# Optimization experiments

Hardware: AMD Instinct MI355X
Metric: run time of the kernel (lower is better)

The kernel has to match this reference:

```python
import jax, jax.numpy as jnp
import numpy as np

B, S, D, H, DK, F, K = 8, 1024, 512, 8, 64, 2048, 31
EPS = 1e-5


def _ln(x, g, b):
    m = jnp.mean(x, -1, keepdims=True)
    v = jnp.mean((x - m) ** 2, -1, keepdims=True)
    return (x - m) * jax.lax.rsqrt(v + EPS) * g + b


def _ff(x, w1, b1, w2, b2):
    return jnp.maximum(x @ w1 + b1, 0.0) @ w2 + b2


def setup_inputs() -> dict:
    key = jax.random.key(0)
    ks = jax.random.split(key, 16)
    w = lambda k, shape: jax.random.normal(k, shape, dtype=jnp.float32) * 0.02
    inp = {"x": jax.random.normal(ks[0], (B, S, D), dtype=jnp.float32)}
    for name in ["norm1", "norm2", "norm3", "norm4", "conv_ln"]:
        inp[name + "_g"] = jnp.ones((D,), jnp.float32)
        inp[name + "_b"] = jnp.zeros((D,), jnp.float32)
    # feed-forward 1 and 2
    inp["ff1_w1"] = w(ks[1], (D, F)); inp["ff1_b1"] = jnp.zeros((F,), jnp.float32)
    inp["ff1_w2"] = w(ks[2], (F, D)); inp["ff1_b2"] = jnp.zeros((D,), jnp.float32)
    inp["ff2_w1"] = w(ks[3], (D, F)); inp["ff2_b1"] = jnp.zeros((F,), jnp.float32)
    inp["ff2_w2"] = w(ks[4], (F, D)); inp["ff2_b2"] = jnp.zeros((D,), jnp.float32)
    # attention projections ([in, out] layout)
    inp["wq"] = w(ks[5], (D, D)); inp["bq"] = jnp.zeros((D,), jnp.float32)
    inp["wk"] = w(ks[6], (D, D)); inp["bk"] = jnp.zeros((D,), jnp.float32)
    inp["wv"] = w(ks[7], (D, D)); inp["bv"] = jnp.zeros((D,), jnp.float32)
    inp["wo"] = w(ks[8], (D, D)); inp["bo"] = jnp.zeros((D,), jnp.float32)
    # convolution module
    inp["pw1_w"] = w(ks[9], (D, 2 * D)); inp["pw1_b"] = jnp.zeros((2 * D,), jnp.float32)
    inp["dw_w"] = w(ks[10], (D, 1, K)); inp["dw_b"] = jnp.zeros((D,), jnp.float32)
    inp["bn_g"] = jnp.ones((D,), jnp.float32); inp["bn_b"] = jnp.zeros((D,), jnp.float32)
    inp["bn_mean"] = jnp.zeros((D,), jnp.float32); inp["bn_var"] = jnp.ones((D,), jnp.float32)
    inp["pw2_w"] = w(ks[11], (D, D)); inp["pw2_b"] = jnp.zeros((D,), jnp.float32)
    return inp


def _forward(x, norm1_g, norm1_b, norm2_g, norm2_b, norm3_g, norm3_b, norm4_g, norm4_b,
             ff1_w1, ff1_b1, ff1_w2, ff1_b2, wq, bq, wk, bk, wv, bv, wo, bo,
             conv_ln_g, conv_ln_b, pw1_w, pw1_b, dw_w, dw_b,
             bn_g, bn_b, bn_mean, bn_var, pw2_w, pw2_b,
             ff2_w1, ff2_b1, ff2_w2, ff2_b2):
    b, s, _ = x.shape
    # half-step FF1
    x = x + 0.5 * _ff(_ln(x, norm1_g, norm1_b), ff1_w1, ff1_b1, ff1_w2, ff1_b2)
    # multi-head self-attention (pre-norm)
    h = _ln(x, norm2_g, norm2_b)
    q = (h @ wq + bq).reshape(b, s, H, DK)
    k = (h @ wk + bk).reshape(b, s, H, DK)
    v = (h @ wv + bv).reshape(b, s, H, DK)
    scores = jnp.einsum("bqhd,bkhd->bhqk", q, k) / jnp.sqrt(jnp.asarray(DK, x.dtype))
    attn = jax.nn.softmax(scores, axis=-1)
    o = jnp.einsum("bhqk,bkhd->bqhd", attn, v).reshape(b, s, D)
    x = x + (o @ wo + bo)
    # convolution module (pre-norm)
    h = _ln(x, norm3_g, norm3_b)
    h = _ln(h, conv_ln_g, conv_ln_b)
    h = h @ pw1_w + pw1_b                                 # [B,S,2D] pointwise conv1
    h = h[..., :D] * jax.nn.sigmoid(h[..., D:])           # GLU over channels
    h = h.transpose(0, 2, 1)                              # [B,D,S]
    h = jax.lax.conv_general_dilated(
        h, dw_w, window_strides=(1,), padding=((K // 2, K // 2),),
        feature_group_count=D, dimension_numbers=("NCH", "OIH", "NCH")) + dw_b[:, None]
    h = (h - bn_mean[:, None]) * jax.lax.rsqrt(bn_var + EPS)[:, None] * bn_g[:, None] + bn_b[:, None]
    h = h * jax.nn.sigmoid(h)                             # SiLU
    h = jnp.einsum("bcl,co->bol", h, pw2_w) + pw2_b[:, None]
    x = x + h.transpose(0, 2, 1)
    # half-step FF2
    x = x + 0.5 * _ff(_ln(x, norm4_g, norm4_b), ff2_w1, ff2_b1, ff2_w2, ff2_b2)
    return x


def reference(x, norm1_g, norm1_b, norm2_g, norm2_b, norm3_g, norm3_b, norm4_g, norm4_b,
              conv_ln_g, conv_ln_b, ff1_w1, ff1_b1, ff1_w2, ff1_b2,
              ff2_w1, ff2_b1, ff2_w2, ff2_b2, wq, bq, wk, bk, wv, bv, wo, bo,
              pw1_w, pw1_b, dw_w, dw_b, bn_g, bn_b, bn_mean, bn_var, pw2_w, pw2_b):
    return _forward(x, norm1_g, norm1_b, norm2_g, norm2_b, norm3_g, norm3_b, norm4_g, norm4_b,
                    ff1_w1, ff1_b1, ff1_w2, ff1_b2, wq, bq, wk, bk, wv, bv, wo, bo,
                    conv_ln_g, conv_ln_b, pw1_w, pw1_b, dw_w, dw_b,
                    bn_g, bn_b, bn_mean, bn_var, pw2_w, pw2_b,
                    ff2_w1, ff2_b1, ff2_w2, ff2_b2)
```

## Files before the change

### kernel.cpp

```cpp
#include <hip/hip_runtime.h>
#include <math.h>

#define TOK    8192
#define DMODEL 512
#define FDIM   2048
#define NH     8
#define DKH    64
#define SEQ    1024
#define BATCH  8
#define KCONV  31
#define LN_EPS 1e-5f

typedef __attribute__((ext_vector_type(8))) short bf16x8;
typedef __attribute__((ext_vector_type(4))) float f32x4;
typedef unsigned short ushort_t;

#define AS1 __attribute__((address_space(1)))
#define AS3 __attribute__((address_space(3)))

__device__ __forceinline__ float sigf(float x) { return 1.0f / (1.0f + __expf(-x)); }

__device__ __forceinline__ unsigned short f2bf(float f) {
  unsigned u = __float_as_uint(f);
  u = u + 0x7fffu + ((u >> 16) & 1u);
  return (unsigned short)(u >> 16);
}
__device__ __forceinline__ unsigned pk2(float a, float b) {
  return (unsigned)f2bf(a) | ((unsigned)f2bf(b) << 16);
}
__device__ __forceinline__ float bf2f(ushort_t u) {
  return __uint_as_float((unsigned)u << 16);
}

__device__ __forceinline__ void xcd_swizzle(int gx, int* bx, int* by) {
  const int nwg = gx * (int)gridDim.y;
  const int cpx = nwg >> 3;
  const int bid = (*by) * gx + (*bx);
  const int wg = (bid & 7) * cpx + (bid >> 3);
  *bx = wg % gx;
  *by = wg / gx;
}

struct WJob { const float* src; ushort_t* dst; int K, N, t0; };
struct WJobs {
  WJob j[10];
  int misc_t0;
  const float* dww; const float* bq; const float* bk; const float* bv;
  float* wTc; float* bcat;
};

__global__ __launch_bounds__(256) void wcast_all(WJobs jobs) {
  __shared__ float tile[32][33];
  const int t = blockIdx.x;
  const int tx = threadIdx.x, ty = threadIdx.y;
  if (t >= jobs.misc_t0) {
    const int idx = (t - jobs.misc_t0) * 256 + ty * 32 + tx;
    if (idx < DMODEL * KCONV) {
      const int d = idx / KCONV, k = idx % KCONV;
      jobs.wTc[k * DMODEL + d] = jobs.dww[idx];
    } else if (idx < DMODEL * KCONV + 3 * DMODEL) {
      const int c = idx - DMODEL * KCONV;
      jobs.bcat[c] = (c < DMODEL) ? jobs.bq[c]
                    : (c < 2 * DMODEL ? jobs.bk[c - DMODEL] : jobs.bv[c - 2 * DMODEL]);
    }
    return;
  }
  int i = 0;
#pragma unroll
  for (int k = 1; k < 10; ++k) if (t >= jobs.j[k].t0) i = k;
  const WJob jb = jobs.j[i];
  const int local = t - jb.t0;
  const int ntx = jb.N >> 5;
  const int bx = (local % ntx) * 32, by = (local / ntx) * 32;
#pragma unroll
  for (int r = 0; r < 32; r += 8)
    tile[ty + r][tx] = jb.src[(size_t)(by + ty + r) * jb.N + bx + tx];
  __syncthreads();
#pragma unroll
  for (int r = 0; r < 32; r += 8)
    jb.dst[(size_t)(bx + ty + r) * jb.K + by + tx] = f2bf(tile[tx][ty + r]);
}

template <bool OBF>
__global__ __launch_bounds__(256) void ln_kernel(const float* __restrict__ in,
                                                 const float* __restrict__ g,
                                                 const float* __restrict__ b,
                                                 void* __restrict__ outp) {
  const int wave = threadIdx.x >> 6, lane = threadIdx.x & 63;
  const size_t row = (size_t)blockIdx.x * 4 + wave;
  const float* p = in + row * DMODEL + lane * 8;
  const float4 v0 = *(const float4*)p;
  const float4 v1 = *(const float4*)(p + 4);
  float s  = v0.x + v0.y + v0.z + v0.w + v1.x + v1.y + v1.z + v1.w;
  float ss = v0.x*v0.x + v0.y*v0.y + v0.z*v0.z + v0.w*v0.w
           + v1.x*v1.x + v1.y*v1.y + v1.z*v1.z + v1.w*v1.w;
#pragma unroll
  for (int m = 1; m < 64; m <<= 1) { s += __shfl_xor(s, m); ss += __shfl_xor(ss, m); }
  const float mean = s * (1.0f / DMODEL);
  const float var  = ss * (1.0f / DMODEL) - mean * mean;
  const float rstd = rsqrtf(var + LN_EPS);
  const float4 g0 = *(const float4*)(g + lane * 8);
  const float4 g1 = *(const float4*)(g + lane * 8 + 4);
  const float4 bb0 = *(const float4*)(b + lane * 8);
  const float4 bb1 = *(const float4*)(b + lane * 8 + 4);
  float o[8];
  o[0] = (v0.x - mean) * rstd * g0.x + bb0.x;
  o[1] = (v0.y - mean) * rstd * g0.y + bb0.y;
  o[2] = (v0.z - mean) * rstd * g0.z + bb0.z;
  o[3] = (v0.w - mean) * rstd * g0.w + bb0.w;
  o[4] = (v1.x - mean) * rstd * g1.x + bb1.x;
  o[5] = (v1.y - mean) * rstd * g1.y + bb1.y;
  o[6] = (v1.z - mean) * rstd * g1.z + bb1.z;
  o[7] = (v1.w - mean) * rstd * g1.w + bb1.w;
  if (OBF) {
    uint4 pkv;
    pkv.x = pk2(o[0], o[1]); pkv.y = pk2(o[2], o[3]);
    pkv.z = pk2(o[4], o[5]); pkv.w = pk2(o[6], o[7]);
    *(uint4*)((ushort_t*)outp + row * DMODEL + lane * 8) = pkv;
  } else {
    float4 a, c;
    a.x = o[0]; a.y = o[1]; a.z = o[2]; a.w = o[3];
    c.x = o[4]; c.y = o[5]; c.z = o[6]; c.w = o[7];
    float* q = (float*)outp + row * DMODEL + lane * 8;
    *(float4*)q = a;
    *(float4*)(q + 4) = c;
  }
}

__global__ __launch_bounds__(256) void ln2_kernel(const float* __restrict__ in,
                                                  const float* __restrict__ g1,
                                                  const float* __restrict__ b1,
                                                  const float* __restrict__ g2,
                                                  const float* __restrict__ b2,
                                                  ushort_t* __restrict__ outp) {
  const int wave = threadIdx.x >> 6, lane = threadIdx.x & 63;
  const size_t row = (size_t)blockIdx.x * 4 + wave;
  const float* p = in + row * DMODEL + lane * 8;
  float v[8];
  {
    const float4 v0 = *(const float4*)p;
    const float4 v1 = *(const float4*)(p + 4);
    v[0]=v0.x; v[1]=v0.y; v[2]=v0.z; v[3]=v0.w;
    v[4]=v1.x; v[5]=v1.y; v[6]=v1.z; v[7]=v1.w;
  }
  float s = 0.f, ss = 0.f;
#pragma unroll
  for (int e = 0; e < 8; ++e) { s += v[e]; ss += v[e]*v[e]; }
#pragma unroll
  for (int m = 1; m < 64; m <<= 1) { s += __shfl_xor(s, m); ss += __shfl_xor(ss, m); }
  float mean = s * (1.0f / DMODEL);
  float rstd = rsqrtf(ss * (1.0f / DMODEL) - mean * mean + LN_EPS);
  const float4 ga = *(const float4*)(g1 + lane * 8);
  const float4 gb = *(const float4*)(g1 + lane * 8 + 4);
  const float4 ba = *(const float4*)(b1 + lane * 8);
  const float4 bb = *(const float4*)(b1 + lane * 8 + 4);
  const float gg1[8] = {ga.x,ga.y,ga.z,ga.w,gb.x,gb.y,gb.z,gb.w};
  const float bb1[8] = {ba.x,ba.y,ba.z,ba.w,bb.x,bb.y,bb.z,bb.w};
#pragma unroll
  for (int e = 0; e < 8; ++e) v[e] = (v[e] - mean) * rstd * gg1[e] + bb1[e];
  s = 0.f; ss = 0.f;
#pragma unroll
  for (int e = 0; e < 8; ++e) { s += v[e]; ss += v[e]*v[e]; }
#pragma unroll
  for (int m = 1; m < 64; m <<= 1) { s += __shfl_xor(s, m); ss += __shfl_xor(ss, m); }
  mean = s * (1.0f / DMODEL);
  rstd = rsqrtf(ss * (1.0f / DMODEL) - mean * mean + LN_EPS);
  const float4 gc = *(const float4*)(g2 + lane * 8);
  const float4 gd = *(const float4*)(g2 + lane * 8 + 4);
  const float4 bc = *(const float4*)(b2 + lane * 8);
  const float4 bd = *(const float4*)(b2 + lane * 8 + 4);
  const float gg2[8] = {gc.x,gc.y,gc.z,gc.w,gd.x,gd.y,gd.z,gd.w};
  const float bb2[8] = {bc.x,bc.y,bc.z,bc.w,bd.x,bd.y,bd.z,bd.w};
  float o[8];
#pragma unroll
  for (int e = 0; e < 8; ++e) o[e] = (v[e] - mean) * rstd * gg2[e] + bb2[e];
  uint4 pkv;
  pkv.x = pk2(o[0], o[1]); pkv.y = pk2(o[2], o[3]);
  pkv.z = pk2(o[4], o[5]); pkv.w = pk2(o[6], o[7]);
  *(uint4*)(outp + row * DMODEL + lane * 8) = pkv;
}

template <int ACT, bool QSC>
__global__ __launch_bounds__(512, 2) void gemm256(const ushort_t* __restrict__ A,
                                                  const ushort_t* __restrict__ Bt,
                                                  const float* __restrict__ bias,
                                                  ushort_t* __restrict__ Cout,
                                                  int N) {
  __shared__ ushort_t lds[65536];
  const int t = threadIdx.x;
  const int l = t & 63;
  const int wid = t >> 6;
  const int wm = wid >> 2, wn = wid & 3;
  int bx = blockIdx.x, by = blockIdx.y;
  xcd_swizzle(gridDim.x, &bx, &by);
  const int m0 = by * 256, n0 = bx * 256;
  const int K = 512;

  f32x4 acc[8][4];
#pragma unroll
  for (int m = 0; m < 8; ++m)
#pragma unroll
    for (int n = 0; n < 4; ++n) acc[m][n] = (f32x4){0.f, 0.f, 0.f, 0.f};

  const int srow = t >> 3;
  const int schunk = (t & 7) ^ ((t >> 3) & 7);

#define STAGE_A(TAU, C_, I_)                                                    \
  __builtin_amdgcn_global_load_lds(                                             \
      (const AS1 unsigned*)(A + (size_t)(m0 + (I_) * 64 + srow) * K +           \
                            (TAU) * 64 + schunk * 8),                           \
      (AS3 unsigned*)(lds + (C_) * 16384 + ((I_) * 512 + t) * 8), 16, 0, 0)
#define STAGE_B(TAU, C_, I_)                                                    \
  __builtin_amdgcn_global_load_lds(                                             \
      (const AS1 unsigned*)(Bt + (size_t)(n0 + (I_) * 64 + srow) * K +          \
                            (TAU) * 64 + schunk * 8),                           \
      (AS3 unsigned*)(lds + 32768 + (C_) * 16384 + ((I_) * 512 + t) * 8), 16, 0, 0)

#pragma unroll
  for (int i = 0; i < 4; ++i) STAGE_B(0, 0, i);
#pragma unroll
  for (int i = 0; i < 4; ++i) STAGE_A(0, 0, i);
#pragma unroll
  for (int i = 0; i < 4; ++i) STAGE_B(1, 1, i);
  STAGE_A(1, 1, 0);
  STAGE_A(1, 1, 2);
  asm volatile("s_waitcnt vmcnt(6)" ::: "memory");
  __builtin_amdgcn_s_barrier();

  const int arow = (l & 15);
  const int kch0 = (l >> 4);
  bf16x8 bfr[2][4];

  for (int it = 0; it < 4; ++it) {
    const bool stg = (it < 3);
#pragma unroll
    for (int h = 0; h < 2; ++h) {
      const int c = h;
#pragma unroll
      for (int p = 0; p < 4; ++p) {
        bf16x8 afr[2][2];
#pragma unroll
        for (int m2 = 0; m2 < 2; ++m2)
#pragma unroll
          for (int ks = 0; ks < 2; ++ks) {
            const int row = wm * 128 + (2 * p + m2) * 16 + arow;
            const int ch = (ks * 4 + kch0) ^ (row & 7);
            afr[m2][ks] = *(const bf16x8*)(lds + c * 16384 + row * 64 + ch * 8);
          }
        if (p == 0) {
#pragma unroll
          for (int nr = 0; nr < 4; ++nr)
#pragma unroll
            for (int ks = 0; ks < 2; ++ks) {
              const int row = wn * 64 + nr * 16 + arow;
              const int ch = (ks * 4 + kch0) ^ (row & 7);
              bfr[ks][nr] = *(const bf16x8*)(lds + 32768 + c * 16384 + row * 64 + ch * 8);
            }
        }
        if (p == 0) {
          if (h == 0 || stg) {
            STAGE_A(2 * it + h + 1, c ^ 1, 1);
            STAGE_A(2 * it + h + 1, c ^ 1, 3);
          }
        } else if (p == 1) {
          if (stg) {
#pragma unroll
            for (int i = 0; i < 4; ++i) STAGE_B(2 * it + h + 2, c, i);
          }
        } else if (p == 2) {
          if (stg) {
            STAGE_A(2 * it + h + 2, c, 0);
            STAGE_A(2 * it + h + 2, c, 2);
          }
        }
        __builtin_amdgcn_s_barrier();
        __builtin_amdgcn_s_setprio(1);
#pragma unroll
        for (int ks = 0; ks < 2; ++ks)
#pragma unroll
          for (int m2 = 0; m2 < 2; ++m2)
#pragma unroll
            for (int nr = 0; nr < 4; ++nr)
              acc[2 * p + m2][nr] = __builtin_amdgcn_mfma_f32_16x16x32_bf16(
                  afr[m2][ks], bfr[ks][nr], acc[2 * p + m2][nr], 0, 0, 0);
        __builtin_amdgcn_s_setprio(0);
        if (p == 3) {
          if (h == 0) {
            if (stg) asm volatile("s_waitcnt vmcnt(6)" ::: "memory");
            else     asm volatile("s_waitcnt vmcnt(0)" ::: "memory");
          } else if (stg) {
            asm volatile("s_waitcnt vmcnt(6)" ::: "memory");
          }
        }
        __builtin_amdgcn_s_barrier();
      }
    }
  }
#undef STAGE_A
#undef STAGE_B

#pragma unroll
  for (int m = 0; m < 8; ++m) {
    const int row_b = m0 + wm * 128 + m * 16 + (l >> 4) * 4;
#pragma unroll
    for (int n = 0; n < 4; ++n) {
      const int col = n0 + wn * 64 + n * 16 + (l & 15);
      const float bv = bias[col];
      const float sc = QSC ? (col < DMODEL ? 0.125f : 1.0f) : 1.0f;
#pragma unroll
      for (int j = 0; j < 4; ++j) {
        float v = acc[m][n][j] + bv;
        if (ACT == 1) v = fmaxf(v, 0.f);
        v *= sc;
        Cout[(size_t)(row_b + j) * N + col] = f2bf(v);
      }
    }
  }
}

template <int TN, int ACT, bool RES, bool OBF, bool QSC>
__global__ __launch_bounds__(256) void gemm_bf16(const ushort_t* __restrict__ A,
                                                 const ushort_t* __restrict__ Bt,
                                                 const float* __restrict__ bias,
                                                 const float* __restrict__ Rp,
                                                 float alpha,
                                                 void* __restrict__ Cout,
                                                 int M, int N, int K) {
  constexpr int NF = TN / 32;
  constexpr int NB = TN / 32;
  __shared__ ushort_t Al[128 * 64];
  __shared__ ushort_t Bl[TN * 64];
  const int t = threadIdx.x;
  const int lane = t & 63;
  const int wid = t >> 6;
  const int wr = wid >> 1, wc = wid & 1;
  int bx = blockIdx.x, by = blockIdx.y;
  xcd_swizzle(gridDim.x, &bx, &by);
  const int m0 = by * 128, n0 = bx * TN;

  f32x4 acc[4][NF];
#pragma unroll
  for (int m = 0; m < 4; ++m)
#pragma unroll
    for (int n = 0; n < NF; ++n) acc[m][n] = (f32x4){0.f, 0.f, 0.f, 0.f};

  const int srow = t >> 3;
  const int scol = (t & 7) * 8;
  const ushort_t* Ag = A + (size_t)(m0 + srow) * K + scol;
  const ushort_t* Bg = Bt + (size_t)(n0 + srow) * K + scol;

  for (int k0 = 0; k0 < K; k0 += 64) {
    __syncthreads();
#pragma unroll
    for (int i = 0; i < 4; ++i) {
      __builtin_amdgcn_global_load_lds(
          (const AS1 unsigned*)(Ag + (size_t)i * 32 * K + k0),
          (AS3 unsigned*)(Al + ((size_t)i * 256 + t) * 8),
          16, 0, 0);
    }
#pragma unroll
    for (int i = 0; i < NB; ++i) {
      __builtin_amdgcn_global_load_lds(
          (const AS1 unsigned*)(Bg + (size_t)i * 32 * K + k0),
          (AS3 unsigned*)(Bl + ((size_t)i * 256 + t) * 8),
          16, 0, 0);
    }
    __syncthreads();

#pragma unroll
    for (int ks = 0; ks < 2; ++ks) {
      const int kk = ks * 32 + (lane >> 4) * 8;
      bf16x8 af[4], bfv[NF];
#pragma unroll
      for (int m = 0; m < 4; ++m)
        af[m] = *(const bf16x8*)(Al + (wr * 64 + m * 16 + (lane & 15)) * 64 + kk);
#pragma unroll
      for (int n = 0; n < NF; ++n)
        bfv[n] = *(const bf16x8*)(Bl + (wc * (TN / 2) + n * 16 + (lane & 15)) * 64 + kk);
#pragma unroll
      for (int m = 0; m < 4; ++m)
#pragma unroll
        for (int n = 0; n < NF; ++n)
          acc[m][n] = __builtin_amdgcn_mfma_f32_16x16x32_bf16(af[m], bfv[n], acc[m][n], 0, 0, 0);
    }
  }

#pragma unroll
  for (int m = 0; m < 4; ++m) {
    const int row_b = m0 + wr * 64 + m * 16 + (lane >> 4) * 4;
#pragma unroll
    for (int n = 0; n < NF; ++n) {
      const int col = n0 + wc * (TN / 2) + n * 16 + (lane & 15);
      const float bv = bias[col];
#pragma unroll
      for (int j = 0; j < 4; ++j) {
        float v = acc[m][n][j] + bv;
        if (ACT == 1) v = fmaxf(v, 0.f);
        if (QSC) v *= (col < DMODEL ? 0.125f : 1.0f);
        const size_t idx = (size_t)(row_b + j) * N + col;
        if (RES) v = Rp[idx] + alpha * v;
        if (OBF) ((ushort_t*)Cout)[idx] = f2bf(v);
        else     ((float*)Cout)[idx] = v;
      }
    }
  }
}

__global__ __launch_bounds__(256) void gemm_glu(const ushort_t* __restrict__ A,
                                                const ushort_t* __restrict__ Bt,
                                                const float* __restrict__ bias,
                                                ushort_t* __restrict__ Cout) {
  __shared__ ushort_t Al[128 * 64];
  __shared__ ushort_t Bl[128 * 64];
  const int t = threadIdx.x;
  const int lane = t & 63;
  const int wid = t >> 6;
  const int wr = wid >> 1, wc = wid & 1;
  int bx = blockIdx.x, by = blockIdx.y;
  xcd_swizzle(gridDim.x, &bx, &by);
  const int m0 = by * 128, n0 = bx * 64;
  const int K = DMODEL, N = DMODEL;

  f32x4 aa[4][2], ag[4][2];
#pragma unroll
  for (int m = 0; m < 4; ++m)
#pragma unroll
    for (int n = 0; n < 2; ++n) {
      aa[m][n] = (f32x4){0.f, 0.f, 0.f, 0.f};
      ag[m][n] = (f32x4){0.f, 0.f, 0.f, 0.f};
    }

  const int srow = t >> 3;
  const int scol = (t & 7) * 8;
  const ushort_t* Ag_ = A + (size_t)(m0 + srow) * K + scol;
  const ushort_t* Ba_ = Bt + (size_t)(n0 + srow) * K + scol;
  const ushort_t* Bg_ = Bt + (size_t)(512 + n0 + srow) * K + scol;

  for (int k0 = 0; k0 < K; k0 += 64) {
    __syncthreads();
#pragma unroll
    for (int i = 0; i < 4; ++i) {
      __builtin_amdgcn_global_load_lds(
          (const AS1 unsigned*)(Ag_ + (size_t)i * 32 * K + k0),
          (AS3 unsigned*)(Al + ((size_t)i * 256 + t) * 8),
          16, 0, 0);
    }
#pragma unroll
    for (int i = 0; i < 2; ++i) {
      __builtin_amdgcn_global_load_lds(
          (const AS1 unsigned*)(Ba_ + (size_t)i * 32 * K + k0),
          (AS3 unsigned*)(Bl + ((size_t)i * 256 + t) * 8),
          16, 0, 0);
      __builtin_amdgcn_global_load_lds(
          (const AS1 unsigned*)(Bg_ + (size_t)i * 32 * K + k0),
          (AS3 unsigned*)(Bl + 64 * 64 + ((size_t)i * 256 + t) * 8),
          16, 0, 0);
    }
    __syncthreads();

#pragma unroll
    for (int ks = 0; ks < 2; ++ks) {
      const int kk = ks * 32 + (lane >> 4) * 8;
      bf16x8 af[4], bfa[2], bfg[2];
#pragma unroll
      for (int m = 0; m < 4; ++m)
        af[m] = *(const bf16x8*)(Al + (wr * 64 + m * 16 + (lane & 15)) * 64 + kk);
#pragma unroll
      for (int n = 0; n < 2; ++n) {
        bfa[n] = *(const bf16x8*)(Bl + (wc * 32 + n * 16 + (lane & 15)) * 64 + kk);
        bfg[n] = *(const bf16x8*)(Bl + (64 + wc * 32 + n * 16 + (lane & 15)) * 64 + kk);
      }
#pragma unroll
      for (int m = 0; m < 4; ++m)
#pragma unroll
        for (int n = 0; n < 2; ++n) {
          aa[m][n] = __builtin_amdgcn_mfma_f32_16x16x32_bf16(af[m], bfa[n], aa[m][n], 0, 0, 0);
          ag[m][n] = __builtin_amdgcn_mfma_f32_16x16x32_bf16(af[m], bfg[n], ag[m][n], 0, 0, 0);
        }
    }
  }

#pragma unroll
  for (int m = 0; m < 4; ++m) {
    const int row_b = m0 + wr * 64 + m * 16 + (lane >> 4) * 4;
#pragma unroll
    for (int n = 0; n < 2; ++n) {
      const int col = n0 + wc * 32 + n * 16 + (lane & 15);
      const float ba_v = bias[col];
      const float bg_v = bias[col + DMODEL];
#pragma unroll
      for (int j = 0; j < 4; ++j) {
        const float av = aa[m][n][j] + ba_v;
        const float gv = ag[m][n][j] + bg_v;
        Cout[(size_t)(row_b + j) * N + col] = f2bf(av * sigf(gv));
      }
    }
  }
}

__global__ __launch_bounds__(256) void vtrans(const ushort_t* __restrict__ QKV,
                                              ushort_t* __restrict__ Vt) {
  __shared__ ushort_t tl[64][72];
  const int st = blockIdx.x;
  const int bh = blockIdx.y;
  const int b = bh >> 3, h = bh & 7;
  const int t = threadIdx.x;
#pragma unroll
  for (int i = 0; i < 2; ++i) {
    const int chunk = i * 256 + t;
    const int sr = chunk >> 3, c8 = (chunk & 7) * 8;
    *(uint4*)&tl[sr][c8] =
        *(const uint4*)(QKV + ((size_t)(b * SEQ + st * 64 + sr) * (3 * DMODEL)) + 2 * DMODEL + h * DKH + c8);
  }
  __syncthreads();
#pragma unroll
  for (int i = 0; i < 2; ++i) {
    const int chunk = i * 256 + t;
    const int dr = chunk >> 3, c8 = (chunk & 7) * 8;
    ushort_t tmp[8];
#pragma unroll
    for (int e = 0; e < 8; ++e) tmp[e] = tl[c8 + e][dr];
    *(uint4*)(Vt + ((size_t)(bh * DKH + dr) * SEQ) + st * 64 + c8) = *(uint4*)tmp;
  }
}

__global__ __launch_bounds__(256) void attn_mfma(const ushort_t* __restrict__ QKV,
                                                 const ushort_t* __restrict__ Vt,
                                                 ushort_t* __restrict__ Om) {
  __shared__ ushort_t Ks[128 * 64];
  __shared__ ushort_t Vs[64 * 128];
  __shared__ ushort_t Ps[64 * 128];
  const int t = threadIdx.x;
  const int l = t & 63;
  const int w = t >> 6;
  const int qb = blockIdx.x, h = blockIdx.y, b = blockIdx.z;
  const size_t rowstr = 3 * DMODEL;
  const size_t baseQ = ((size_t)b * SEQ) * rowstr + (size_t)h * DKH;
  const size_t baseK = baseQ + DMODEL;
  const size_t baseV = (size_t)(b * NH + h) * DKH * SEQ;
  const size_t baseO = ((size_t)b * SEQ) * DMODEL + (size_t)h * DKH;

  bf16x8 qf[2];
  {
    const int qrow = qb * 64 + w * 16 + (l & 15);
    const ushort_t* qp = QKV + baseQ + (size_t)qrow * rowstr + ((l >> 4) * 8);
    qf[0] = *(const bf16x8*)(qp);
    qf[1] = *(const bf16x8*)(qp + 32);
  }

  const int krr = t >> 3, kch = t & 7;
  const int vrr = t >> 4, vch = t & 15;

  float mrun[4], lrun[4];
  f32x4 o[4];
#pragma unroll
  for (int j = 0; j < 4; ++j) { mrun[j] = -1e30f; lrun[j] = 0.f; }
#pragma unroll
  for (int n = 0; n < 4; ++n) o[n] = (f32x4){0.f, 0.f, 0.f, 0.f};

  for (int kt = 0; kt < SEQ / 128; ++kt) {
    __syncthreads();
#pragma unroll
    for (int i = 0; i < 4; ++i) {
      const int r = i * 32 + krr;
      __builtin_amdgcn_global_load_lds(
          (const AS1 unsigned*)
              (QKV + baseK + (size_t)(kt * 128 + r) * rowstr + ((kch ^ (r & 7)) * 8)),
          (AS3 unsigned*)(Ks + ((size_t)i * 256 + t) * 8),
          16, 0, 0);
    }
#pragma unroll
    for (int i = 0; i < 4; ++i) {
      const int r = i * 16 + vrr;
      __builtin_amdgcn_global_load_lds(
          (const AS1 unsigned*)
              (Vt + baseV + (size_t)r * SEQ + kt * 128 + ((vch ^ (r & 15)) * 8)),
          (AS3 unsigned*)(Vs + ((size_t)i * 256 + t) * 8),
          16, 0, 0);
    }
    __syncthreads();

    f32x4 s[8];
#pragma unroll
    for (int n = 0; n < 8; ++n) s[n] = (f32x4){0.f, 0.f, 0.f, 0.f};
    __builtin_amdgcn_s_setprio(1);
#pragma unroll
    for (int ks = 0; ks < 2; ++ks) {
      const int kk = ks * 64 + (l >> 4) * 16;
#pragma unroll
      for (int n = 0; n < 8; ++n) {
        const int krow = n * 16 + (l & 15);
        const bf16x8 kf = *(const bf16x8*)((char*)Ks + krow * 128 + (kk ^ ((krow & 7) << 4)));
        s[n] = __builtin_amdgcn_mfma_f32_16x16x32_bf16(qf[ks], kf, s[n], 0, 0, 0);
      }
    }
    __builtin_amdgcn_s_setprio(0);

#pragma unroll
    for (int j = 0; j < 4; ++j) {
      float r0 = s[0][j];
#pragma unroll
      for (int n = 1; n < 8; ++n) r0 = fmaxf(r0, s[n][j]);
      r0 = fmaxf(r0, __shfl_xor(r0, 1));
      r0 = fmaxf(r0, __shfl_xor(r0, 2));
      r0 = fmaxf(r0, __shfl_xor(r0, 4));
      r0 = fmaxf(r0, __shfl_xor(r0, 8));
      const float mn = fmaxf(mrun[j], r0);
      const float cs = __expf(mrun[j] - mn);
      const int prow = w * 16 + (l >> 4) * 4 + j;
      const int pswz = (prow & 15) << 4;
      float psum = 0.f;
#pragma unroll
      for (int n = 0; n < 8; ++n) {
        const float p = __expf(s[n][j] - mn);
        psum += p;
        const int col2 = (n * 16 + (l & 15)) * 2;
        *(ushort_t*)((char*)Ps + prow * 256 + (col2 ^ pswz)) = f2bf(p);
      }
      psum += __shfl_xor(psum, 1);
      psum += __shfl_xor(psum, 2);
      psum += __shfl_xor(psum, 4);
      psum += __shfl_xor(psum, 8);
      lrun[j] = lrun[j] * cs + psum;
      mrun[j] = mn;
      o[0][j] *= cs; o[1][j] *= cs; o[2][j] *= cs; o[3][j] *= cs;
    }

    __builtin_amdgcn_s_setprio(1);
#pragma unroll
    for (int ks = 0; ks < 4; ++ks) {
      const int kk = ks * 64 + (l >> 4) * 16;
      const int arow = w * 16 + (l & 15);
      const bf16x8 pf = *(const bf16x8*)((char*)Ps + arow * 256 + (kk ^ ((arow & 15) << 4)));
#pragma unroll
      for (int n = 0; n < 4; ++n) {
        const int vrow = n * 16 + (l & 15);
        const bf16x8 vf = *(const bf16x8*)((char*)Vs + vrow * 256 + (kk ^ ((vrow & 15) << 4)));
        o[n] = __builtin_amdgcn_mfma_f32_16x16x32_bf16(pf, vf, o[n], 0, 0, 0);
      }
    }
    __builtin_amdgcn_s_setprio(0);
  }

  float inv[4];
#pragma unroll
  for (int j = 0; j < 4; ++j) inv[j] = 1.0f / lrun[j];
#pragma unroll
  for (int j = 0; j < 4; ++j) {
    const int prow = w * 16 + (l >> 4) * 4 + j;
    const int pswz = (prow & 15) << 4;
#pragma unroll
    for (int n = 0; n < 4; ++n) {
      const int col2 = (n * 16 + (l & 15)) * 2;
      *(ushort_t*)((char*)Ps + prow * 256 + (col2 ^ pswz)) = f2bf(o[n][j] * inv[j]);
    }
  }
  __syncthreads();
#pragma unroll
  for (int i = 0; i < 2; ++i) {
    const int chunk = i * 256 + t;
    const int qr = chunk >> 3, c8 = (chunk & 7) * 8;
    const uint4 ov = *(const uint4*)((char*)Ps + qr * 256 + ((c8 * 2) ^ ((qr & 15) << 4)));
    *(uint4*)(Om + baseO + (size_t)(qb * 64 + qr) * DMODEL + c8) = ov;
  }
}

__global__ __launch_bounds__(256) void dwconv_bn_silu(const ushort_t* __restrict__ in,
                                                      const float* __restrict__ wT,
                                                      const float* __restrict__ dwb,
                                                      const float* __restrict__ bng,
                                                      const float* __restrict__ bnb,
                                                      const float* __restrict__ bnm,
                                                      const float* __restrict__ bnv,
                                                      ushort_t* __restrict__ out) {
  const size_t gid = (size_t)blockIdx.x * 256 + threadIdx.x;
  const int dc = (int)(gid & 127) * 4;
  const int s = (int)((gid >> 7) & (SEQ - 1));
  const int b = (int)(gid >> 17);
  const ushort_t* bp = in + (size_t)b * SEQ * DMODEL;
  float ax = 0.f, ay = 0.f, az = 0.f, aw = 0.f;
#pragma unroll
  for (int k = 0; k < KCONV; ++k) {
    const int ssi = s + k - (KCONV / 2);
    if (ssi < 0 || ssi >= SEQ) continue;
    ushort_t xv[4];
    *(uint2*)xv = *(const uint2*)(bp + (size_t)ssi * DMODEL + dc);
    const float4 w = *(const float4*)(wT + k * DMODEL + dc);
    ax = fmaf(bf2f(xv[0]), w.x, ax); ay = fmaf(bf2f(xv[1]), w.y, ay);
    az = fmaf(bf2f(xv[2]), w.z, az); aw = fmaf(bf2f(xv[3]), w.w, aw);
  }
  const float4 bi = *(const float4*)(dwb + dc);
  const float4 mm = *(const float4*)(bnm + dc);
  const float4 vv = *(const float4*)(bnv + dc);
  const float4 gg = *(const float4*)(bng + dc);
  const float4 b2 = *(const float4*)(bnb + dc);
  float v0 = ax + bi.x, v1 = ay + bi.y, v2 = az + bi.z, v3 = aw + bi.w;
  v0 = (v0 - mm.x) * rsqrtf(vv.x + LN_EPS) * gg.x + b2.x;
  v1 = (v1 - mm.y) * rsqrtf(vv.y + LN_EPS) * gg.y + b2.y;
  v2 = (v2 - mm.z) * rsqrtf(vv.z + LN_EPS) * gg.z + b2.z;
  v3 = (v3 - mm.w) * rsqrtf(vv.w + LN_EPS) * gg.w + b2.w;
  v0 = v0 * sigf(v0); v1 = v1 * sigf(v1); v2 = v2 * sigf(v2); v3 = v3 * sigf(v3);
  uint2 o;
  o.x = pk2(v0, v1); o.y = pk2(v2, v3);
  *(uint2*)&out[(((size_t)b * SEQ + s) * DMODEL) + dc] = o;
}

extern "C" void kernel_launch(void* const* d_in, const int* in_sizes, int n_in,
                              void* d_out, int out_size, void* d_ws, size_t ws_size,
                              hipStream_t stream) {
  const float* x    = (const float*)d_in[0];
  const float* n1g  = (const float*)d_in[1];
  const float* n1b  = (const float*)d_in[2];
  const float* n2g  = (const float*)d_in[3];
  const float* n2b  = (const float*)d_in[4];
  const float* n3g  = (const float*)d_in[5];
  const float* n3b  = (const float*)d_in[6];
  const float* n4g  = (const float*)d_in[7];
  const float* n4b  = (const float*)d_in[8];
  const float* clg  = (const float*)d_in[9];
  const float* clb  = (const float*)d_in[10];
  const float* f1w1 = (const float*)d_in[11];
  const float* f1b1 = (const float*)d_in[12];
  const float* f1w2 = (const float*)d_in[13];
  const float* f1b2 = (const float*)d_in[14];
  const float* f2w1 = (const float*)d_in[15];
  const float* f2b1 = (const float*)d_in[16];
  const float* f2w2 = (const float*)d_in[17];
  const float* f2b2 = (const float*)d_in[18];
  const float* wq   = (const float*)d_in[19];
  const float* bq   = (const float*)d_in[20];
  const float* wk   = (const float*)d_in[21];
  const float* bk   = (const float*)d_in[22];
  const float* wv   = (const float*)d_in[23];
  const float* bv   = (const float*)d_in[24];
  const float* wo   = (const float*)d_in[25];
  const float* bo   = (const float*)d_in[26];
  const float* pw1w = (const float*)d_in[27];
  const float* pw1b = (const float*)d_in[28];
  const float* dww  = (const float*)d_in[29];
  const float* dwb  = (const float*)d_in[30];
  const float* bng  = (const float*)d_in[31];
  const float* bnb  = (const float*)d_in[32];
  const float* bnm  = (const float*)d_in[33];
  const float* bnv  = (const float*)d_in[34];
  const float* pw2w = (const float*)d_in[35];
  const float* pw2b = (const float*)d_in[36];

  char* wsb = (char*)d_ws;
  const size_t MB = 1ull << 20;
  ushort_t* Wbf    = (ushort_t*)(wsb + 0);
  ushort_t* f1w1T  = Wbf + 0;
  ushort_t* f1w2T  = Wbf + (1ull << 20);
  ushort_t* f2w1T  = Wbf + (2ull << 20);
  ushort_t* f2w2T  = Wbf + (3ull << 20);
  ushort_t* wqkvT  = Wbf + (4ull << 20);
  ushort_t* wkT    = wqkvT + (256ull << 10);
  ushort_t* wvT    = wqkvT + (512ull << 10);
  ushort_t* woT    = wqkvT + (768ull << 10);
  ushort_t* pw1T   = Wbf + (5ull << 20);
  ushort_t* pw2T   = Wbf + (5ull << 20) + (512ull << 10);
  float*    WTc    = (float*)(wsb + 12 * MB);
  float*    bcat   = (float*)(wsb + 12 * MB + 128 * 1024);
  ushort_t* Lbf    = (ushort_t*)(wsb + 13 * MB);
  ushort_t* Hbf    = (ushort_t*)(wsb + 21 * MB);
  ushort_t* QKVb   = (ushort_t*)(wsb + 53 * MB);
  ushort_t* Vtb    = (ushort_t*)(wsb + 77 * MB);
  ushort_t* Gbf    = (ushort_t*)(wsb + 53 * MB);
  ushort_t* Obf    = (ushort_t*)(wsb + 85 * MB);
  ushort_t* Cbf    = Obf;
  float* out = (float*)d_out;

  const dim3 blk(256);
  const dim3 blk512(512);
  const dim3 blkT(32, 8);
  const dim3 gLN(TOK / 4);
  const dim3 gFFa256(FDIM / 256, TOK / 256);
  const dim3 gQKV256(3 * DMODEL / 256, TOK / 256);
  const dim3 gFFb(DMODEL / 64, TOK / 128);
  const dim3 gGLU(DMODEL / 64, TOK / 128);
  const dim3 gAttn(SEQ / 64, NH, BATCH);
  const dim3 gVt(SEQ / 64, BATCH * NH);
  const dim3 gElem(TOK * 128 / 256);

  {
    WJobs jobs;
    const float* srcs[10] = {f1w1, f1w2, f2w1, f2w2, wq, wk, wv, wo, pw1w, pw2w};
    ushort_t* dsts[10] = {f1w1T, f1w2T, f2w1T, f2w2T, wqkvT, wkT, wvT, woT, pw1T, pw2T};
    const int Ks[10] = {512, 2048, 512, 2048, 512, 512, 512, 512, 512, 512};
    const int Ns[10] = {2048, 512, 2048, 512, 512, 512, 512, 512, 1024, 512};
    int t0 = 0;
    for (int i = 0; i < 10; ++i) {
      jobs.j[i].src = srcs[i]; jobs.j[i].dst = dsts[i];
      jobs.j[i].K = Ks[i]; jobs.j[i].N = Ns[i]; jobs.j[i].t0 = t0;
      t0 += (Ks[i] / 32) * (Ns[i] / 32);
    }
    jobs.misc_t0 = t0;
    jobs.dww = dww; jobs.bq = bq; jobs.bk = bk; jobs.bv = bv;
    jobs.wTc = WTc; jobs.bcat = bcat;
    const int nmisc = (DMODEL * KCONV + 3 * DMODEL + 255) / 256;
    wcast_all<<<t0 + nmisc, blkT, 0, stream>>>(jobs);
  }

  ln_kernel<true><<<gLN, blk, 0, stream>>>(x, n1g, n1b, Lbf);
  gemm256<1, false><<<gFFa256, blk512, 0, stream>>>(Lbf, f1w1T, f1b1, Hbf, FDIM);
  gemm_bf16<64,  0, true,  false, false><<<gFFb, blk, 0, stream>>>(Hbf, f1w2T, f1b2, x, 0.5f, out, TOK, DMODEL, FDIM);

  ln_kernel<true><<<gLN, blk, 0, stream>>>(out, n2g, n2b, Lbf);
  gemm256<0, true><<<gQKV256, blk512, 0, stream>>>(Lbf, wqkvT, bcat, QKVb, 3 * DMODEL);
  vtrans<<<gVt, blk, 0, stream>>>(QKVb, Vtb);
  attn_mfma<<<gAttn, blk, 0, stream>>>(QKVb, Vtb, Obf);
  gemm_bf16<64,  0, true,  false, false><<<gFFb, blk, 0, stream>>>(Obf, woT, bo, out, 1.0f, out, TOK, DMODEL, DMODEL);

  ln2_kernel<<<gLN, blk, 0, stream>>>(out, n3g, n3b, clg, clb, Lbf);
  gemm_glu<<<gGLU, blk, 0, stream>>>(Lbf, pw1T, pw1b, Gbf);
  dwconv_bn_silu<<<gElem, blk, 0, stream>>>(Gbf, WTc, dwb, bng, bnb, bnm, bnv, Cbf);
  gemm_bf16<64,  0, true,  false, false><<<gFFb, blk, 0, stream>>>(Cbf, pw2T, pw2b, out, 1.0f, out, TOK, DMODEL, DMODEL);

  ln_kernel<true><<<gLN, blk, 0, stream>>>(out, n4g, n4b, Lbf);
  gemm256<1, false><<<gFFa256, blk512, 0, stream>>>(Lbf, f2w1T, f2b1, Hbf, FDIM);
  gemm_bf16<64,  0, true,  false, false><<<gFFb, blk, 0, stream>>>(Hbf, f2w2T, f2b2, out, 0.5f, out, TOK, DMODEL, FDIM);
}
```

Baseline: 312.4 us.

## Read attention K/V fragments straight from global memory with XCD-aware block order

Measured after the change: 401.4 us. +28.5%, slower.

```diff
diff --git a/kernel.cpp b/kernel.cpp
--- a/kernel.cpp
+++ b/kernel.cpp
@@ -17,6 +17,8 @@
 
 #define AS1 __attribute__((address_space(1)))
 #define AS3 __attribute__((address_space(3)))
+
+#define QSCALE 0.1803368801111204f
 
 __device__ __forceinline__ float sigf(float x) { return 1.0f / (1.0f + __expf(-x)); }
 
@@ -306,7 +308,7 @@
     for (int n = 0; n < 4; ++n) {
       const int col = n0 + wn * 64 + n * 16 + (l & 15);
       const float bv = bias[col];
-      const float sc = QSC ? (col < DMODEL ? 0.125f : 1.0f) : 1.0f;
+      const float sc = QSC ? (col < DMODEL ? QSCALE : 1.0f) : 1.0f;
 #pragma unroll
       for (int j = 0; j < 4; ++j) {
         float v = acc[m][n][j] + bv;
@@ -396,7 +398,7 @@
       for (int j = 0; j < 4; ++j) {
         float v = acc[m][n][j] + bv;
         if (ACT == 1) v = fmaxf(v, 0.f);
-        if (QSC) v *= (col < DMODEL ? 0.125f : 1.0f);
+        if (QSC) v *= (col < DMODEL ? QSCALE : 1.0f);
         const size_t idx = (size_t)(row_b + j) * N + col;
         if (RES) v = Rp[idx] + alpha * v;
         if (OBF) ((ushort_t*)Cout)[idx] = f2bf(v);
@@ -499,6 +501,7 @@
 }
 
 __global__ __launch_bounds__(256) void vtrans(const ushort_t* __restrict__ QKV,
+                                              ushort_t* __restrict__ Kp,
                                               ushort_t* __restrict__ Vt) {
   __shared__ ushort_t tl[64][72];
   const int st = blockIdx.x;
@@ -509,8 +512,10 @@
   for (int i = 0; i < 2; ++i) {
     const int chunk = i * 256 + t;
     const int sr = chunk >> 3, c8 = (chunk & 7) * 8;
-    *(uint4*)&tl[sr][c8] =
-        *(const uint4*)(QKV + ((size_t)(b * SEQ + st * 64 + sr) * (3 * DMODEL)) + 2 * DMODEL + h * DKH + c8);
+    const size_t src = (size_t)(b * SEQ + st * 64 + sr) * (3 * DMODEL) + h * DKH + c8;
+    *(uint4*)&tl[sr][c8] = *(const uint4*)(QKV + src + 2 * DMODEL);
+    *(uint4*)(Kp + ((size_t)(bh * SEQ + st * 64 + sr)) * DKH + c8) =
+        *(const uint4*)(QKV + src + DMODEL);
   }
   __syncthreads();
 #pragma unroll
@@ -525,20 +530,22 @@
 }
 
 __global__ __launch_bounds__(256) void attn_mfma(const ushort_t* __restrict__ QKV,
+                                                 const ushort_t* __restrict__ Kp,
                                                  const ushort_t* __restrict__ Vt,
                                                  ushort_t* __restrict__ Om) {
-  __shared__ ushort_t Ks[128 * 64];
-  __shared__ ushort_t Vs[64 * 128];
   __shared__ ushort_t Ps[64 * 128];
   const int t = threadIdx.x;
   const int l = t & 63;
   const int w = t >> 6;
-  const int qb = blockIdx.x, h = blockIdx.y, b = blockIdx.z;
+  const int bid = blockIdx.x;
+  const int wg = (bid & 7) * 128 + (bid >> 3);
+  const int qb = wg & 15;
+  const int bh = wg >> 4;
   const size_t rowstr = 3 * DMODEL;
-  const size_t baseQ = ((size_t)b * SEQ) * rowstr + (size_t)h * DKH;
-  const size_t baseK = baseQ + DMODEL;
-  const size_t baseV = (size_t)(b * NH + h) * DKH * SEQ;
-  const size_t baseO = ((size_t)b * SEQ) * DMODEL + (size_t)h * DKH;
+  const size_t baseQ  = (size_t)(bh >> 3) * SEQ * rowstr + (size_t)(bh & 7) * DKH;
+  const size_t baseKp = (size_t)bh * SEQ * DKH;
+  const size_t baseV  = (size_t)bh * DKH * SEQ;
+  const size_t baseO  = (size_t)(bh >> 3) * SEQ * DMODEL + (size_t)(bh & 7) * DKH;
 
   bf16x8 qf[2];
   {
@@ -548,9 +555,6 @@
     qf[1] = *(const bf16x8*)(qp + 32);
   }
 
-  const int krr = t >> 3, kch = t & 7;
-  const int vrr = t >> 4, vch = t & 15;
-
   float mrun[4], lrun[4];
   f32x4 o[4];
 #pragma unroll
@@ -559,38 +563,17 @@
   for (int n = 0; n < 4; ++n) o[n] = (f32x4){0.f, 0.f, 0.f, 0.f};
 
   for (int kt = 0; kt < SEQ / 128; ++kt) {
-    __syncthreads();
-#pragma unroll
-    for (int i = 0; i < 4; ++i) {
-      const int r = i * 32 + krr;
-      __builtin_amdgcn_global_load_lds(
-          (const AS1 unsigned*)
-              (QKV + baseK + (size_t)(kt * 128 + r) * rowstr + ((kch ^ (r & 7)) * 8)),
-          (AS3 unsigned*)(Ks + ((size_t)i * 256 + t) * 8),
-          16, 0, 0);
-    }
-#pragma unroll
-    for (int i = 0; i < 4; ++i) {
-      const int r = i * 16 + vrr;
-      __builtin_amdgcn_global_load_lds(
-          (const AS1 unsigned*)
-              (Vt + baseV + (size_t)r * SEQ + kt * 128 + ((vch ^ (r & 15)) * 8)),
-          (AS3 unsigned*)(Vs + ((size_t)i * 256 + t) * 8),
-          16, 0, 0);
-    }
-    __syncthreads();
-
     f32x4 s[8];
 #pragma unroll
     for (int n = 0; n < 8; ++n) s[n] = (f32x4){0.f, 0.f, 0.f, 0.f};
     __builtin_amdgcn_s_setprio(1);
 #pragma unroll
     for (int ks = 0; ks < 2; ++ks) {
-      const int kk = ks * 64 + (l >> 4) * 16;
+      const int koff = ks * 32 + (l >> 4) * 8;
 #pragma unroll
       for (int n = 0; n < 8; ++n) {
-        const int krow = n * 16 + (l & 15);
-        const bf16x8 kf = *(const bf16x8*)((char*)Ks + krow * 128 + (kk ^ ((krow & 7) << 4)));
+        const int krow = kt * 128 + n * 16 + (l & 15);
+        const bf16x8 kf = *(const bf16x8*)(Kp + baseKp + (size_t)krow * DKH + koff);
         s[n] = __builtin_amdgcn_mfma_f32_16x16x32_bf16(qf[ks], kf, s[n], 0, 0, 0);
       }
     }
@@ -598,21 +581,20 @@
 
 #pragma unroll
     for (int j = 0; j < 4; ++j) {
-      float r0 = s[0][j];
-#pragma unroll
-      for (int n = 1; n < 8; ++n) r0 = fmaxf(r0, s[n][j]);
+      float r0 = fmaxf(fmaxf(fmaxf(s[0][j], s[1][j]), fmaxf(s[2][j], s[3][j])),
+                       fmaxf(fmaxf(s[4][j], s[5][j]), fmaxf(s[6][j], s[7][j])));
       r0 = fmaxf(r0, __shfl_xor(r0, 1));
       r0 = fmaxf(r0, __shfl_xor(r0, 2));
       r0 = fmaxf(r0, __shfl_xor(r0, 4));
       r0 = fmaxf(r0, __shfl_xor(r0, 8));
       const float mn = fmaxf(mrun[j], r0);
-      const float cs = __expf(mrun[j] - mn);
+      const float cs = exp2f(mrun[j] - mn);
       const int prow = w * 16 + (l >> 4) * 4 + j;
       const int pswz = (prow & 15) << 4;
       float psum = 0.f;
 #pragma unroll
       for (int n = 0; n < 8; ++n) {
-        const float p = __expf(s[n][j] - mn);
+        const float p = exp2f(s[n][j] - mn);
         psum += p;
         const int col2 = (n * 16 + (l & 15)) * 2;
         *(ushort_t*)((char*)Ps + prow * 256 + (col2 ^ pswz)) = f2bf(p);
@@ -632,10 +614,11 @@
       const int kk = ks * 64 + (l >> 4) * 16;
       const int arow = w * 16 + (l & 15);
       const bf16x8 pf = *(const bf16x8*)((char*)Ps + arow * 256 + (kk ^ ((arow & 15) << 4)));
+      const int voff = kt * 128 + ks * 32 + (l >> 4) * 8;
 #pragma unroll
       for (int n = 0; n < 4; ++n) {
         const int vrow = n * 16 + (l & 15);
-        const bf16x8 vf = *(const bf16x8*)((char*)Vs + vrow * 256 + (kk ^ ((vrow & 15) << 4)));
+        const bf16x8 vf = *(const bf16x8*)(Vt + baseV + (size_t)vrow * SEQ + voff);
         o[n] = __builtin_amdgcn_mfma_f32_16x16x32_bf16(pf, vf, o[n], 0, 0, 0);
       }
     }
@@ -768,6 +751,7 @@
   ushort_t* Gbf    = (ushort_t*)(wsb + 53 * MB);
   ushort_t* Obf    = (ushort_t*)(wsb + 85 * MB);
   ushort_t* Cbf    = Obf;
+  ushort_t* Kpb    = (ushort_t*)(wsb + 93 * MB);
   float* out = (float*)d_out;
 
   const dim3 blk(256);
@@ -778,7 +762,7 @@
   const dim3 gQKV256(3 * DMODEL / 256, TOK / 256);
   const dim3 gFFb(DMODEL / 64, TOK / 128);
   const dim3 gGLU(DMODEL / 64, TOK / 128);
-  const dim3 gAttn(SEQ / 64, NH, BATCH);
+  const dim3 gAttn(BATCH * NH * (SEQ / 64));
   const dim3 gVt(SEQ / 64, BATCH * NH);
   const dim3 gElem(TOK * 128 / 256);
 
@@ -807,8 +791,8 @@
 
   ln_kernel<true><<<gLN, blk, 0, stream>>>(out, n2g, n2b, Lbf);
   gemm256<0, true><<<gQKV256, blk512, 0, stream>>>(Lbf, wqkvT, bcat, QKVb, 3 * DMODEL);
-  vtrans<<<gVt, blk, 0, stream>>>(QKVb, Vtb);
-  attn_mfma<<<gAttn, blk, 0, stream>>>(QKVb, Vtb, Obf);
+  vtrans<<<gVt, blk, 0, stream>>>(QKVb, Kpb, Vtb);
+  attn_mfma<<<gAttn, blk, 0, stream>>>(QKVb, Kpb, Vtb, Obf);
   gemm_bf16<64,  0, true,  false, false><<<gFFb, blk, 0, stream>>>(Obf, woT, bo, out, 1.0f, out, TOK, DMODEL, DMODEL);
 
   ln2_kernel<<<gLN, blk, 0, stream>>>(out, n3g, n3b, clg, clb, Lbf);
```
